# Performance work log

Hardware: AMD Instinct MI355X
Metric: run time of the kernel (lower is better)

Reference implementation:

```python
import jax, jax.numpy as jnp
import numpy as np

# Genome structure (from init_kwargs): ids 0..N_INPUTS-1 are input nodes,
# ids N_NODES-N_OUTPUTS..N_NODES-1 are output nodes.
N_NODES = 32
N_INPUTS = 8
N_OUTPUTS = 4
N_EDGES = 128
BATCH = 524288


def setup_inputs() -> dict:
    key = jax.random.key(0)
    k1, k2, k3, k4 = jax.random.split(key, 4)
    x = jax.random.normal(k1, (N_INPUTS, BATCH), dtype=jnp.float32)
    w = jax.random.normal(k2, (N_EDGES,), dtype=jnp.float32) * 0.5
    src = jax.random.randint(k3, (N_EDGES,), 0, N_NODES, dtype=jnp.int32)
    dst = jax.random.randint(k4, (N_EDGES,), 0, N_NODES, dtype=jnp.int32)
    return {"x": x, "w": w, "src": src, "dst": dst}


def _forward(x, w, src, dst):
    # vals[n] is the [BATCH]-vector state of node n (torch dict-of-scalars, batched).
    vals = jnp.zeros((N_NODES, BATCH), dtype=x.dtype).at[:N_INPUTS].set(x)

    # Faithful to torch: edges are applied SEQUENTIALLY within a sweep
    # (later edges see earlier updates), so use scan, not a parallel scatter.
    def edge_step(v, edge):
        i, o, wv = edge
        return v.at[o].add(jnp.tanh(v[i] * wv)), None

    def iter_body(v, _):
        v, _ = jax.lax.scan(edge_step, v, (src, dst, w))
        return v, None

    # torch: `for _ in range(len(self.g.nodes))` -> N_NODES relaxation sweeps
    vals, _ = jax.lax.scan(iter_body, vals, None, length=N_NODES)

    # torch: stack([tanh(vals[o]) for o in outputs]) -> [N_OUTPUTS, BATCH]
    return jnp.tanh(vals[N_NODES - N_OUTPUTS:])


def reference(x, w, src, dst):
    return _forward(x, w, src, dst)
```

## Files before the change

kernel.cpp:

```cpp
#include <hip/hip_runtime.h>


#define N_NODES   32
#define N_INPUTS  8
#define N_OUTPUTS 4
#define N_EDGES   128
#define BATCH     524288
#define BLOCK     256

#define TWO_LOG2E 2.88539008177792681472f

__device__ __forceinline__ float tanh_from_exp2(float x_times_k) {
    const float u = __builtin_amdgcn_exp2f(x_times_k);
    return 1.0f - 2.0f * __builtin_amdgcn_rcpf(1.0f + u);
}

__global__ __launch_bounds__(BLOCK)
void EvolvedNet_80032420593868_kernel(const float* __restrict__ x,
                                      const float* __restrict__ w,
                                      const int*   __restrict__ src,
                                      const int*   __restrict__ dst,
                                      float*       __restrict__ out) {
    __shared__ float vals[N_NODES][BLOCK];

    const int tid = threadIdx.x;
    const int b   = blockIdx.x * BLOCK + tid;

#pragma unroll
    for (int n = 0; n < N_INPUTS; ++n)
        vals[n][tid] = x[n * BATCH + b];
#pragma unroll
    for (int n = N_INPUTS; n < N_NODES; ++n)
        vals[n][tid] = 0.0f;


    for (int sweep = 0; sweep < N_NODES; ++sweep) {
#pragma unroll 8
        for (int e = 0; e < N_EDGES; ++e) {
            const int   s  = src[e];
            const int   d  = dst[e];
            const float wk = w[e] * TWO_LOG2E;
            const float v  = vals[s][tid];
            const float t  = tanh_from_exp2(v * wk);
            vals[d][tid] += t;
        }
    }

#pragma unroll
    for (int o = 0; o < N_OUTPUTS; ++o) {
        const float v = vals[N_NODES - N_OUTPUTS + o][tid];
        out[o * BATCH + b] = tanh_from_exp2(v * TWO_LOG2E);
    }
}

extern "C" void kernel_launch(void* const* d_in, const int* in_sizes, int n_in,
                              void* d_out, int out_size, void* d_ws, size_t ws_size,
                              hipStream_t stream) {
    const float* x   = (const float*)d_in[0];
    const float* w   = (const float*)d_in[1];
    const int*   src = (const int*)d_in[2];
    const int*   dst = (const int*)d_in[3];
    float*       out = (float*)d_out;

    const int grid = BATCH / BLOCK;
    EvolvedNet_80032420593868_kernel<<<grid, BLOCK, 0, stream>>>(x, w, src, dst, out);
}
```

Before: 642.9 us.

## Process two batch elements per thread with float2 LDS and scalar edge metadata

A small prep kernel precomputes the scaled weights and the src/dst LDS offsets, and readfirstlane keeps them in scalar registers. The main kernel now uses 64-thread blocks, with each thread handling two batch elements stored as float2 in LDS. This halves the per-element cost of loading edge metadata and issuing LDS instructions, and adds independent work per thread for latency hiding. The cost is an extra kernel launch and fewer threads per block, which leaves the scheduler fewer waves to hide latency with.

```diff
diff --git a/kernel.cpp b/kernel.cpp
--- a/kernel.cpp
+++ b/kernel.cpp
@@ -6,50 +6,86 @@
 #define N_OUTPUTS 4
 #define N_EDGES   128
 #define BATCH     524288
-#define BLOCK     256
+#define BLOCK     64
+#define EPT       2
+#define TILE      (BLOCK * EPT)
 
 #define TWO_LOG2E 2.88539008177792681472f
 
-__device__ __forceinline__ float tanh_from_exp2(float x_times_k) {
-    const float u = __builtin_amdgcn_exp2f(x_times_k);
-    return 1.0f - 2.0f * __builtin_amdgcn_rcpf(1.0f + u);
+typedef float f32x2 __attribute__((ext_vector_type(2)));
+
+__device__ __forceinline__ float sread_f(const float* p) {
+    return __int_as_float(__builtin_amdgcn_readfirstlane(__float_as_int(*p)));
+}
+
+__global__ void EvolvedNet_prep(const float* __restrict__ w,
+                                const int*   __restrict__ src,
+                                const int*   __restrict__ dst,
+                                int* __restrict__ soff, int* __restrict__ doff,
+                                float* __restrict__ wk) {
+    const int e = threadIdx.x;
+    if (e < N_EDGES) {
+        soff[e] = src[e] * BLOCK;
+        doff[e] = dst[e] * BLOCK;
+        wk[e]   = w[e] * TWO_LOG2E;
+    }
 }
 
 __global__ __launch_bounds__(BLOCK)
 void EvolvedNet_80032420593868_kernel(const float* __restrict__ x,
-                                      const float* __restrict__ w,
-                                      const int*   __restrict__ src,
-                                      const int*   __restrict__ dst,
+                                      const int*   __restrict__ soff,
+                                      const int*   __restrict__ doff,
+                                      const float* __restrict__ wk,
                                       float*       __restrict__ out) {
-    __shared__ float vals[N_NODES][BLOCK];
+    __shared__ f32x2 vals[N_NODES * BLOCK];
 
     const int tid = threadIdx.x;
-    const int b   = blockIdx.x * BLOCK + tid;
+    const int b0  = blockIdx.x * TILE + tid * 2;
 
 #pragma unroll
     for (int n = 0; n < N_INPUTS; ++n)
-        vals[n][tid] = x[n * BATCH + b];
+        vals[n * BLOCK + tid] = *(const f32x2*)&x[n * BATCH + b0];
 #pragma unroll
     for (int n = N_INPUTS; n < N_NODES; ++n)
-        vals[n][tid] = 0.0f;
+        vals[n * BLOCK + tid] = (f32x2)(0.0f, 0.0f);
 
 
     for (int sweep = 0; sweep < N_NODES; ++sweep) {
 #pragma unroll 8
         for (int e = 0; e < N_EDGES; ++e) {
-            const int   s  = src[e];
-            const int   d  = dst[e];
-            const float wk = w[e] * TWO_LOG2E;
-            const float v  = vals[s][tid];
-            const float t  = tanh_from_exp2(v * wk);
-            vals[d][tid] += t;
+            const int   so = __builtin_amdgcn_readfirstlane(soff[e]);
+            const int   dd = __builtin_amdgcn_readfirstlane(doff[e]);
+            const float wv = sread_f(&wk[e]);
+
+            const f32x2 v = vals[so + tid];
+            f32x2 a; a.x = v.x * wv; a.y = v.y * wv;
+            f32x2 u;
+            u.x = __builtin_amdgcn_exp2f(a.x);
+            u.y = __builtin_amdgcn_exp2f(a.y);
+            f32x2 s1; s1.x = 1.0f + u.x; s1.y = 1.0f + u.y;
+            f32x2 r;
+            r.x = __builtin_amdgcn_rcpf(s1.x);
+            r.y = __builtin_amdgcn_rcpf(s1.y);
+            f32x2 t; t.x = 1.0f - 2.0f * r.x;
+            t.y = 1.0f - 2.0f * r.y;
+
+            f32x2 dv = vals[dd + tid];
+            dv.x += t.x; dv.y += t.y;
+            vals[dd + tid] = dv;
         }
     }
 
 #pragma unroll
     for (int o = 0; o < N_OUTPUTS; ++o) {
-        const float v = vals[N_NODES - N_OUTPUTS + o][tid];
-        out[o * BATCH + b] = tanh_from_exp2(v * TWO_LOG2E);
+        const f32x2 v = vals[(N_NODES - N_OUTPUTS + o) * BLOCK + tid];
+        f32x2 t;
+        {
+            const float ax = v.x * TWO_LOG2E;
+            const float ay = v.y * TWO_LOG2E;
+            t.x = 1.0f - 2.0f * __builtin_amdgcn_rcpf(1.0f + __builtin_amdgcn_exp2f(ax));
+            t.y = 1.0f - 2.0f * __builtin_amdgcn_rcpf(1.0f + __builtin_amdgcn_exp2f(ay));
+        }
+        *(f32x2*)&out[o * BATCH + b0] = t;
     }
 }
 
@@ -62,6 +98,12 @@
     const int*   dst = (const int*)d_in[3];
     float*       out = (float*)d_out;
 
-    const int grid = BATCH / BLOCK;
-    EvolvedNet_80032420593868_kernel<<<grid, BLOCK, 0, stream>>>(x, w, src, dst, out);
+    int*   soff = (int*)d_ws;
+    int*   doff = soff + N_EDGES;
+    float* wkp  = (float*)(doff + N_EDGES);
+
+    EvolvedNet_prep<<<1, 128, 0, stream>>>(w, src, dst, soff, doff, wkp);
+
+    const int grid = BATCH / TILE;
+    EvolvedNet_80032420593868_kernel<<<grid, BLOCK, 0, stream>>>(x, soff, doff, wkp, out);
 }
```

Result: slower. 760.0 us (+18.2%).

## Pack edge table in a prep kernel and broadcast via readlane with unrolled edges

Applied to the files above, without the earlier changes.

A new tiny prep kernel packs each edge's src and dst LDS offsets into one word and pre-scales the weights by 2*log2(e), writing both to workspace. The main kernel loads the 128-edge table into two registers per lane. It then fetches each edge's uniform values with readlane instead of per-edge scalar memory loads. The edge loop is fully unrolled, and the next edge's LDS operands are loaded right after the current store to hide LDS latency. This adds a second launch and a larger code footprint, and it relies on the ws buffer being available.

```diff
diff --git a/kernel.cpp b/kernel.cpp
--- a/kernel.cpp
+++ b/kernel.cpp
@@ -10,46 +10,76 @@
 
 #define TWO_LOG2E 2.88539008177792681472f
 
-__device__ __forceinline__ float tanh_from_exp2(float x_times_k) {
-    const float u = __builtin_amdgcn_exp2f(x_times_k);
-    return 1.0f - 2.0f * __builtin_amdgcn_rcpf(1.0f + u);
+__global__ void EvolvedNet_prep(const float* __restrict__ w,
+                                const int*   __restrict__ src,
+                                const int*   __restrict__ dst,
+                                unsigned* __restrict__ sodo,
+                                float*    __restrict__ wk) {
+    const int e = threadIdx.x;
+    if (e < N_EDGES) {
+        sodo[e] = (unsigned)(src[e] * BLOCK) | ((unsigned)(dst[e] * BLOCK) << 16);
+        wk[e]   = w[e] * TWO_LOG2E;
+    }
 }
+
+#define RLU(arr, E) ((unsigned)__builtin_amdgcn_readlane((int)arr[(E) >> 6], (E) & 63))
+#define RLF(arr, E) __uint_as_float((unsigned)__builtin_amdgcn_readlane( \
+                        (int)__float_as_uint(arr[(E) >> 6]), (E) & 63))
 
 __global__ __launch_bounds__(BLOCK)
 void EvolvedNet_80032420593868_kernel(const float* __restrict__ x,
-                                      const float* __restrict__ w,
-                                      const int*   __restrict__ src,
-                                      const int*   __restrict__ dst,
-                                      float*       __restrict__ out) {
-    __shared__ float vals[N_NODES][BLOCK];
+                                      const unsigned* __restrict__ sodo,
+                                      const float*    __restrict__ wk,
+                                      float*          __restrict__ out) {
+    __shared__ float vals[N_NODES * BLOCK];
 
-    const int tid = threadIdx.x;
-    const int b   = blockIdx.x * BLOCK + tid;
+    const int tid  = threadIdx.x;
+    const int lane = tid & 63;
+    const int b    = blockIdx.x * BLOCK + tid;
+
+    unsigned rsodo[2];
+    float    rwk[2];
+    rsodo[0] = sodo[lane];  rsodo[1] = sodo[lane + 64];
+    rwk[0]   = wk[lane];    rwk[1]   = wk[lane + 64];
 
 #pragma unroll
     for (int n = 0; n < N_INPUTS; ++n)
-        vals[n][tid] = x[n * BATCH + b];
+        vals[n * BLOCK + tid] = x[n * BATCH + b];
 #pragma unroll
     for (int n = N_INPUTS; n < N_NODES; ++n)
-        vals[n][tid] = 0.0f;
+        vals[n * BLOCK + tid] = 0.0f;
 
 
+    unsigned p0 = RLU(rsodo, 0);
+    int   iS = (int)(p0 & 0xFFFFu) + tid;
+    int   iD = (int)(p0 >> 16) + tid;
+    float ps = vals[iS];
+    float pd = vals[iD];
+
     for (int sweep = 0; sweep < N_NODES; ++sweep) {
-#pragma unroll 8
+#pragma unroll
         for (int e = 0; e < N_EDGES; ++e) {
-            const int   s  = src[e];
-            const int   d  = dst[e];
-            const float wk = w[e] * TWO_LOG2E;
-            const float v  = vals[s][tid];
-            const float t  = tanh_from_exp2(v * wk);
-            vals[d][tid] += t;
+            const float wkv = RLF(rwk, e);
+            const float a   = ps * wkv;
+            const float u   = __builtin_amdgcn_exp2f(a);
+            const float rc  = __builtin_amdgcn_rcpf(1.0f + u);
+            const float t   = __builtin_fmaf(-2.0f, rc, 1.0f);
+
+            vals[iD] = pd + t;
+
+            const unsigned pn = RLU(rsodo, (e + 1) & (N_EDGES - 1));
+            iS = (int)(pn & 0xFFFFu) + tid;
+            iD = (int)(pn >> 16) + tid;
+            ps = vals[iS];
+            pd = vals[iD];
         }
     }
 
 #pragma unroll
     for (int o = 0; o < N_OUTPUTS; ++o) {
-        const float v = vals[N_NODES - N_OUTPUTS + o][tid];
-        out[o * BATCH + b] = tanh_from_exp2(v * TWO_LOG2E);
+        const float v = vals[(N_NODES - N_OUTPUTS + o) * BLOCK + tid];
+        const float u = __builtin_amdgcn_exp2f(v * TWO_LOG2E);
+        out[o * BATCH + b] = __builtin_fmaf(-2.0f, __builtin_amdgcn_rcpf(1.0f + u), 1.0f);
     }
 }
 
@@ -62,6 +92,11 @@
     const int*   dst = (const int*)d_in[3];
     float*       out = (float*)d_out;
 
+    unsigned* sodop = (unsigned*)d_ws;
+    float*    wkp   = (float*)(sodop + N_EDGES);
+
+    EvolvedNet_prep<<<1, 128, 0, stream>>>(w, src, dst, sodop, wkp);
+
     const int grid = BATCH / BLOCK;
-    EvolvedNet_80032420593868_kernel<<<grid, BLOCK, 0, stream>>>(x, w, src, dst, out);
+    EvolvedNet_80032420593868_kernel<<<grid, BLOCK, 0, stream>>>(x, sodop, wkp, out);
 }
```

Result: slower. 698.6 us (+8.7%).
